# Optimization experiments

Hardware: AMD Instinct MI355X
Metric: run time of the kernel (lower is better)

## Reference

```python
import jax, jax.numpy as jnp
import numpy as np

SIZE_IN = 4096
SIZE_OUT = 4096
BATCH = 4096


def setup_inputs() -> dict:
    key = jax.random.key(0)
    k1, k2, k3, k4, k5, k6 = jax.random.split(key, 6)
    mu_in = jax.random.normal(k1, (BATCH, SIZE_IN), dtype=jnp.float32)
    sigma_in = jax.random.uniform(k2, (BATCH, SIZE_IN), dtype=jnp.float32)
    # parameters, initialized as in the torch module
    w_mu = 5e-05 * jax.random.normal(k3, (SIZE_IN, SIZE_OUT), dtype=jnp.float32)
    w_sigma = jax.random.uniform(k4, (SIZE_IN * SIZE_OUT,), dtype=jnp.float32,
                                 minval=-12.0, maxval=-2.2)
    b_mu = 5e-05 * jax.random.normal(k5, (SIZE_OUT,), dtype=jnp.float32)
    b_sigma = jax.random.uniform(k6, (SIZE_OUT,), dtype=jnp.float32,
                                 minval=-12.0, maxval=-10.0)
    return {"mu_in": mu_in, "sigma_in": sigma_in, "w_mu": w_mu,
            "w_sigma": w_sigma, "b_mu": b_mu, "b_sigma": b_sigma}


def reference(mu_in, sigma_in, w_mu, w_sigma, b_mu, b_sigma):
    # mean path: mu_out[b,o] = sum_i mu_in[b,i] * w_mu[i,o] + b_mu[o]
    mu_out = jnp.einsum('bi,io->bo', mu_in, w_mu) + b_mu
    # variance path: x diag(softplus(w_sigma)) x^T, per output feature.
    # Equivalent to (mu_in^2) @ softplus(w_sigma).reshape(size_in, size_out),
    # avoiding the quadratic diag_embed + bmm materialization.
    sigma_w = jax.nn.softplus(w_sigma).reshape(SIZE_IN, SIZE_OUT)
    Sigma_out = jnp.einsum('bi,io->bo', mu_in * mu_in, sigma_w) + jax.nn.softplus(b_sigma)
    # KL loss, verbatim from the torch code
    sp = jax.nn.softplus(w_sigma)
    term1 = SIZE_IN * jnp.log(sp)
    term2 = jnp.sum(jnp.abs(w_mu))
    term3 = SIZE_IN * sp
    kl_loss = -0.5 * jnp.mean(term1 - term2 - term3)
    return (mu_out, Sigma_out, kl_loss)
```

## Files before the change

### kernel.cpp

```cpp
#include <hip/hip_runtime.h>
#include <hip/hip_bf16.h>
#include <math.h>

#define M_BATCH   4096
#define K_IN      4096
#define N_OUT     4096
#define NELEM     16777216

typedef __bf16 bf16;
typedef bf16  bf16x8 __attribute__((ext_vector_type(8)));
typedef float f32x4  __attribute__((ext_vector_type(4)));

__device__ __forceinline__ float softplus_fast(float x) {
    if (x > 15.f) return x;
    const float e = __expf(x);
    if (e < 0.0883f)
        return e * (1.f + e * (-0.5f + e * 0.3333333f));
    return __logf(1.f + e);
}

__device__ __forceinline__ unsigned short f2bf_bits(float x) {
    bf16 b = (bf16)x;
    return __builtin_bit_cast(unsigned short, b);
}

__device__ __forceinline__ void gload_lds16(const void* g, void* l) {
    __builtin_amdgcn_global_load_lds(
        (__attribute__((address_space(1))) void*)g,
        (__attribute__((address_space(3))) void*)l,
        16, 0, 0);
}

__global__ __launch_bounds__(256) void prep_a(const float4* __restrict__ mu,
                                              ushort4* __restrict__ A,
                                              ushort4* __restrict__ A2) {
    const int i = blockIdx.x * 256 + threadIdx.x;
    const float4 v = mu[i];
    ushort4 a, a2;
    a.x  = f2bf_bits(v.x);       a.y  = f2bf_bits(v.y);
    a.z  = f2bf_bits(v.z);       a.w  = f2bf_bits(v.w);
    a2.x = f2bf_bits(v.x * v.x); a2.y = f2bf_bits(v.y * v.y);
    a2.z = f2bf_bits(v.z * v.z); a2.w = f2bf_bits(v.w * v.w);
    A[i]  = a;
    A2[i] = a2;
}

__global__ __launch_bounds__(256) void prep_w(const float* __restrict__ wmu,
                                              const float* __restrict__ wsg,
                                              bf16* __restrict__ Wmu_t,
                                              bf16* __restrict__ Wsg_t,
                                              float* __restrict__ partials) {
    __shared__ bf16 tmu[64][65];
    __shared__ bf16 tsg[64][65];
    __shared__ float red[256];

    const int t  = threadIdx.x;
    const int ti = blockIdx.y;
    const int tj = blockIdx.x;
    const int r  = t >> 4;
    const int c4 = (t & 15) << 2;

    float s_abs = 0.f, s_sp = 0.f, s_log = 0.f;

    for (int rr = 0; rr < 64; rr += 16) {
        const int row = rr + r;
        const size_t goff = (size_t)(ti * 64 + row) * N_OUT + tj * 64 + c4;
        const float4 vm = *(const float4*)(wmu + goff);
        const float4 vs = *(const float4*)(wsg + goff);
        const float sp0 = softplus_fast(vs.x), sp1 = softplus_fast(vs.y);
        const float sp2 = softplus_fast(vs.z), sp3 = softplus_fast(vs.w);
        s_abs += fabsf(vm.x) + fabsf(vm.y) + fabsf(vm.z) + fabsf(vm.w);
        s_sp  += sp0 + sp1 + sp2 + sp3;
        s_log += __logf(sp0) + __logf(sp1) + __logf(sp2) + __logf(sp3);
        tmu[row][c4 + 0] = (bf16)vm.x; tmu[row][c4 + 1] = (bf16)vm.y;
        tmu[row][c4 + 2] = (bf16)vm.z; tmu[row][c4 + 3] = (bf16)vm.w;
        tsg[row][c4 + 0] = (bf16)sp0;  tsg[row][c4 + 1] = (bf16)sp1;
        tsg[row][c4 + 2] = (bf16)sp2;  tsg[row][c4 + 3] = (bf16)sp3;
    }
    __syncthreads();

    for (int cc = 0; cc < 64; cc += 16) {
        const int j  = cc + r;
        const int i0 = c4;
        ushort4 om, os;
        om.x = __builtin_bit_cast(unsigned short, tmu[i0 + 0][j]);
        om.y = __builtin_bit_cast(unsigned short, tmu[i0 + 1][j]);
        om.z = __builtin_bit_cast(unsigned short, tmu[i0 + 2][j]);
        om.w = __builtin_bit_cast(unsigned short, tmu[i0 + 3][j]);
        os.x = __builtin_bit_cast(unsigned short, tsg[i0 + 0][j]);
        os.y = __builtin_bit_cast(unsigned short, tsg[i0 + 1][j]);
        os.z = __builtin_bit_cast(unsigned short, tsg[i0 + 2][j]);
        os.w = __builtin_bit_cast(unsigned short, tsg[i0 + 3][j]);
        const size_t o = (size_t)(tj * 64 + j) * K_IN + ti * 64 + i0;
        *(ushort4*)(Wmu_t + o) = om;
        *(ushort4*)(Wsg_t + o) = os;
    }

    const int bid = blockIdx.y * 64 + blockIdx.x;
    float vals[3] = { s_log, s_sp, s_abs };
    for (int v = 0; v < 3; v++) {
        __syncthreads();
        red[t] = vals[v];
        __syncthreads();
        for (int s = 128; s > 0; s >>= 1) {
            if (t < s) red[t] += red[t + s];
            __syncthreads();
        }
        if (t == 0) partials[v * 4096 + bid] = red[0];
    }
}

#define MFMA_BF16 __builtin_amdgcn_mfma_f32_16x16x32_bf16

__global__ __launch_bounds__(512, 2) void gemm_bf16(
    const bf16* __restrict__ A1,  const bf16* __restrict__ Bt1,
    const float* __restrict__ bias1, float* __restrict__ C1,
    const bf16* __restrict__ A2_, const bf16* __restrict__ Bt2,
    const float* __restrict__ bias2, float* __restrict__ C2) {

    __shared__ bf16 As[2 * 256 * 64];
    __shared__ bf16 Bs[2 * 256 * 64];

    const int z = blockIdx.z;
    const bf16*  A    = z ? A2_   : A1;
    const bf16*  Bt   = z ? Bt2   : Bt1;
    const float* bias = z ? bias2 : bias1;
    float*       C    = z ? C2    : C1;

    const int t = threadIdx.x;
    const int id   = blockIdx.y * 16 + blockIdx.x;
    const int xcd  = id & 7, cc_ = id >> 3;
    const int rowBase = (((xcd >> 1) << 2) + (cc_ >> 3)) << 8;
    const int colBase = (((xcd & 1) << 3) + (cc_ & 7)) << 8;

    const int srow   = t >> 3;
    const int schunk = (t & 7) ^ (srow & 7);
    const char* aG = (const char*)(A  + (size_t)(rowBase + srow) * K_IN + schunk * 8);
    const char* bG = (const char*)(Bt + (size_t)(colBase + srow) * K_IN + schunk * 8);
    char* aL = (char*)As + t * 16;
    char* bL = (char*)Bs + t * 16;

#define STAGE_A(kt, h, par) do {                                               \
        const size_t kb_ = (size_t)((kt) & 63) << 7;                           \
        gload_lds16(aG + kb_ + (size_t)(h) * (128 * K_IN * 2),                 \
                    aL + ((par) << 15) + ((h) << 14));                         \
        gload_lds16(aG + kb_ + (size_t)(h) * (128 * K_IN * 2) + 64 * K_IN * 2, \
                    aL + ((par) << 15) + ((h) << 14) + 8192);                  \
    } while (0)
#define STAGE_B(kt, h, par) do {                                               \
        const size_t kb_ = (size_t)((kt) & 63) << 7;                           \
        gload_lds16(bG + kb_ + (size_t)(h) * (128 * K_IN * 2),                 \
                    bL + ((par) << 15) + ((h) << 14));                         \
        gload_lds16(bG + kb_ + (size_t)(h) * (128 * K_IN * 2) + 64 * K_IN * 2, \
                    bL + ((par) << 15) + ((h) << 14) + 8192);                  \
    } while (0)

    const int lane = t & 63;
    const int wave = t >> 6;
    const int wr = wave >> 2;
    const int wc = wave & 3;
    const int frow = lane & 15;
    const int blk0 = (lane >> 4) ^ (lane & 7);
    const int c0 = blk0 << 4;
    const int c1 = (blk0 ^ 4) << 4;
    const char* aRd = (const char*)As + ((wr << 7) + frow) * 128;
    const char* bRd = (const char*)Bs + ((wc << 6) + frow) * 128;

#define DS_A(par, fi, ck) (*(const bf16x8*)(aRd + ((par) << 15) + ((fi) << 11) + (ck)))
#define DS_B(par, n,  ck) (*(const bf16x8*)(bRd + ((par) << 15) + ((n)  << 11) + (ck)))

#define PHASE(par, q, STAGE_STMT, VM, BAR) do {                                   \
        if ((q) == 0) {                                                           \
            _Pragma("unroll")                                                     \
            for (int n = 0; n < 4; ++n) {                                         \
                bfrag[n][0] = DS_B(par, n, c0);                                   \
                bfrag[n][1] = DS_B(par, n, c1);                                   \
            }                                                                     \
        }                                                                         \
        const bf16x8 a0k0 = DS_A(par, (q) * 2 + 0, c0);                           \
        const bf16x8 a0k1 = DS_A(par, (q) * 2 + 0, c1);                           \
        const bf16x8 a1k0 = DS_A(par, (q) * 2 + 1, c0);                           \
        const bf16x8 a1k1 = DS_A(par, (q) * 2 + 1, c1);                           \
        STAGE_STMT;                                                               \
        __builtin_amdgcn_s_setprio(1);                                            \
        _Pragma("unroll")                                                         \
        for (int n = 0; n < 4; ++n) {          \
            acc[(q)*2+0][n] = MFMA_BF16(a0k0, bfrag[n][0], acc[(q)*2+0][n],0,0,0);\
            acc[(q)*2+1][n] = MFMA_BF16(a1k0, bfrag[n][0], acc[(q)*2+1][n],0,0,0);\
        }                                                                         \
        _Pragma("unroll")                                                         \
        for (int n = 0; n < 4; ++n) {               \
            acc[(q)*2+0][n] = MFMA_BF16(a0k1, bfrag[n][1], acc[(q)*2+0][n],0,0,0);\
            acc[(q)*2+1][n] = MFMA_BF16(a1k1, bfrag[n][1], acc[(q)*2+1][n],0,0,0);\
        }                                                                         \
        __builtin_amdgcn_s_setprio(0);                                            \
        if (VM) {                                                                 \
            asm volatile("s_waitcnt vmcnt(4)" ::: "memory");                      \
            __builtin_amdgcn_sched_barrier(0);                                    \
        }                                                                         \
        if (BAR) {                                                                \
            __builtin_amdgcn_sched_barrier(0);                                    \
            __builtin_amdgcn_s_barrier();                                         \
            __builtin_amdgcn_sched_barrier(0);                                    \
        }                                                                         \
    } while (0)

    const f32x4 zero = { 0.f, 0.f, 0.f, 0.f };
    f32x4 acc[8][4];
#pragma unroll
    for (int m = 0; m < 8; ++m)
#pragma unroll
        for (int n = 0; n < 4; ++n) acc[m][n] = zero;

    STAGE_A(0, 0, 0); STAGE_A(0, 1, 0);
    STAGE_B(0, 0, 0); STAGE_B(0, 1, 0);
    STAGE_A(1, 0, 1); STAGE_A(1, 1, 1);
    STAGE_B(1, 0, 1); STAGE_B(1, 1, 1);
    asm volatile("s_waitcnt vmcnt(8)" ::: "memory");
    __builtin_amdgcn_sched_barrier(0);
    __builtin_amdgcn_s_barrier();
    __builtin_amdgcn_sched_barrier(0);

    for (int i = 0; i < 32; ++i) {
        const int kA1 = 2 * i + 1;
        const int kB0 = 2 * i + 2;
        const int kA0 = 2 * i + 2;
        const int kB1 = 2 * i + 3;
        {
            bf16x8 bfrag[4][2];
            PHASE(0, 0, STAGE_A(kA1, 0, 1), 0, 0);
            PHASE(0, 1, STAGE_A(kA1, 1, 1), 0, 1);
            PHASE(0, 2, STAGE_B(kB0, 0, 0), 0, 0);
            PHASE(0, 3, STAGE_B(kB0, 1, 0), 1, 1);
        }
        {
            bf16x8 bfrag[4][2];
            PHASE(1, 0, STAGE_A(kA0, 0, 0), 0, 0);
            PHASE(1, 1, STAGE_A(kA0, 1, 0), 0, 1);
            PHASE(1, 2, STAGE_B(kB1, 0, 1), 0, 0);
            PHASE(1, 3, STAGE_B(kB1, 1, 1), 1, 1);
        }
    }

    asm volatile("s_waitcnt vmcnt(0)" ::: "memory");

    const int r0 = (lane >> 4) << 2;
    const int ccol = colBase + (wc << 6) + (lane & 15);
#pragma unroll
    for (int n = 0; n < 4; ++n) {
        const int c = ccol + n * 16;
        float b = bias[c];
        if (z) b = softplus_fast(b);
#pragma unroll
        for (int m = 0; m < 8; ++m) {
            const int rbase = rowBase + (wr << 7) + (m << 4) + r0;
#pragma unroll
            for (int reg = 0; reg < 4; ++reg)
                C[(size_t)(rbase + reg) * N_OUT + c] = acc[m][n][reg] + b;
        }
    }
#undef STAGE_A
#undef STAGE_B
#undef DS_A
#undef DS_B
#undef PHASE
}

__global__ __launch_bounds__(256) void kl_finish(const float* __restrict__ partials,
                                                 const int n,
                                                 float* __restrict__ out) {
    __shared__ double red[256];
    const int t = threadIdx.x;
    double sums[3];
    for (int v = 0; v < 3; v++) {
        double a = 0.0;
        for (int i = t; i < n; i += 256) a += (double)partials[v * n + i];
        red[t] = a;
        __syncthreads();
        for (int s = 128; s > 0; s >>= 1) {
            if (t < s) red[t] += red[t + s];
            __syncthreads();
        }
        sums[v] = red[0];
        __syncthreads();
    }
    if (t == 0) {
        const double mean_log = sums[0] / 16777216.0;
        const double mean_sp  = sums[1] / 16777216.0;
        const double kl = -0.5 * (4096.0 * mean_log - sums[2] - 4096.0 * mean_sp);
        out[0] = (float)kl;
    }
}

__global__ void fb_partials(const float* __restrict__ wmu,
                            const float* __restrict__ wsg,
                            float* __restrict__ partials) {
    __shared__ float red[256];
    const int t = threadIdx.x;
    float s_abs = 0.f, s_sp = 0.f, s_log = 0.f;
    for (int i = blockIdx.x * 256 + t; i < NELEM; i += 1024 * 256) {
        s_abs += fabsf(wmu[i]);
        const float sp = softplus_fast(wsg[i]);
        s_sp += sp;
        s_log += __logf(sp);
    }
    float vals[3] = { s_log, s_sp, s_abs };
    for (int v = 0; v < 3; v++) {
        __syncthreads();
        red[t] = vals[v];
        __syncthreads();
        for (int s = 128; s > 0; s >>= 1) {
            if (t < s) red[t] += red[t + s];
            __syncthreads();
        }
        if (t == 0) partials[v * 1024 + blockIdx.x] = red[0];
    }
}

__global__ void fb_gemm(const float* __restrict__ A,
                        const float* __restrict__ Wm,
                        const float* __restrict__ Ws,
                        const float* __restrict__ bmu,
                        const float* __restrict__ bsg,
                        float* __restrict__ Cmu,
                        float* __restrict__ Csg) {
    __shared__ float As_[16][17], Bm[16][17], Bs_[16][17];
    const int tx = threadIdx.x, ty = threadIdx.y;
    const int row = blockIdx.y * 16 + ty;
    const int col = blockIdx.x * 16 + tx;
    float am = 0.f, as = 0.f;
    for (int k0 = 0; k0 < K_IN; k0 += 16) {
        As_[ty][tx] = A[(size_t)row * K_IN + k0 + tx];
        Bm[ty][tx]  = Wm[(size_t)(k0 + ty) * N_OUT + col];
        Bs_[ty][tx] = softplus_fast(Ws[(size_t)(k0 + ty) * N_OUT + col]);
        __syncthreads();
#pragma unroll
        for (int kk = 0; kk < 16; kk++) {
            const float av = As_[ty][kk];
            am += av * Bm[kk][tx];
            as += av * av * Bs_[kk][tx];
        }
        __syncthreads();
    }
    Cmu[(size_t)row * N_OUT + col] = am + bmu[col];
    Csg[(size_t)row * N_OUT + col] = as + softplus_fast(bsg[col]);
}

extern "C" void kernel_launch(void* const* d_in, const int* in_sizes, int n_in,
                              void* d_out, int out_size, void* d_ws, size_t ws_size,
                              hipStream_t stream) {
    const float* mu_in   = (const float*)d_in[0];
    const float* w_mu    = (const float*)d_in[2];
    const float* w_sigma = (const float*)d_in[3];
    const float* b_mu    = (const float*)d_in[4];
    const float* b_sigma = (const float*)d_in[5];

    float* out_mu  = (float*)d_out;
    float* out_sig = out_mu + (size_t)NELEM;
    float* out_kl  = out_mu + 2 * (size_t)NELEM;

    const size_t mat  = (size_t)NELEM;
    const size_t need = mat * 2 * 4  + 3 * 4096 * sizeof(float);

    if (ws_size >= need) {
        bf16* A      = (bf16*)d_ws;
        bf16* A2     = A + mat;
        bf16* Wmu_t  = A2 + mat;
        bf16* Wsg_t  = Wmu_t + mat;
        float* parts = (float*)(Wsg_t + mat);

        prep_a<<<NELEM / 4 / 256, 256, 0, stream>>>(
            (const float4*)mu_in, (ushort4*)A, (ushort4*)A2);
        prep_w<<<dim3(64, 64), 256, 0, stream>>>(
            w_mu, w_sigma, Wmu_t, Wsg_t, parts);
        gemm_bf16<<<dim3(16, 16, 2), 512, 0, stream>>>(
            A, Wmu_t, b_mu, out_mu, A2, Wsg_t, b_sigma, out_sig);
        kl_finish<<<1, 256, 0, stream>>>(parts, 4096, out_kl);
    } else {
        float* parts = (float*)d_ws;
        fb_partials<<<1024, 256, 0, stream>>>(w_mu, w_sigma, parts);
        fb_gemm<<<dim3(256, 256), dim3(16, 16), 0, stream>>>(
            mu_in, w_mu, w_sigma, b_mu, b_sigma, out_mu, out_sig);
        kl_finish<<<1, 256, 0, stream>>>(parts, 1024, out_kl);
    }
}
```

Before: 575.7 us.

## Switch GEMM to 32x32x16 MFMA and merge prep kernels into one launch

The GEMM inner loop moves from 16x16x32 bf16 MFMA tiles to 32x32x16 tiles. This halves the instruction count per tile and changes the LDS fragment reads and swizzle to match the new operand layout. The two prep kernels (activation cast and weight transpose/softplus) become one launch with the blocks split by index, and the block reduction now uses wavefront shuffles instead of a shared-memory tree. The risk is LDS bank conflicts under the new swizzle and strided epilogue stores.

```diff
diff --git a/kernel.cpp b/kernel.cpp
--- a/kernel.cpp
+++ b/kernel.cpp
@@ -10,6 +10,7 @@
 typedef __bf16 bf16;
 typedef bf16  bf16x8 __attribute__((ext_vector_type(8)));
 typedef float f32x4  __attribute__((ext_vector_type(4)));
+typedef float f32x16 __attribute__((ext_vector_type(16)));
 
 __device__ __forceinline__ float softplus_fast(float x) {
     if (x > 15.f) return x;
@@ -31,32 +32,40 @@
         16, 0, 0);
 }
 
-__global__ __launch_bounds__(256) void prep_a(const float4* __restrict__ mu,
-                                              ushort4* __restrict__ A,
-                                              ushort4* __restrict__ A2) {
-    const int i = blockIdx.x * 256 + threadIdx.x;
-    const float4 v = mu[i];
-    ushort4 a, a2;
-    a.x  = f2bf_bits(v.x);       a.y  = f2bf_bits(v.y);
-    a.z  = f2bf_bits(v.z);       a.w  = f2bf_bits(v.w);
-    a2.x = f2bf_bits(v.x * v.x); a2.y = f2bf_bits(v.y * v.y);
-    a2.z = f2bf_bits(v.z * v.z); a2.w = f2bf_bits(v.w * v.w);
-    A[i]  = a;
-    A2[i] = a2;
-}
-
-__global__ __launch_bounds__(256) void prep_w(const float* __restrict__ wmu,
-                                              const float* __restrict__ wsg,
-                                              bf16* __restrict__ Wmu_t,
-                                              bf16* __restrict__ Wsg_t,
-                                              float* __restrict__ partials) {
+__global__ __launch_bounds__(256) void prep_all(const float* __restrict__ wmu,
+                                                const float* __restrict__ wsg,
+                                                bf16* __restrict__ Wmu_t,
+                                                bf16* __restrict__ Wsg_t,
+                                                float* __restrict__ partials,
+                                                const float4* __restrict__ mu,
+                                                ushort4* __restrict__ A,
+                                                ushort4* __restrict__ A2) {
     __shared__ bf16 tmu[64][65];
     __shared__ bf16 tsg[64][65];
-    __shared__ float red[256];
-
-    const int t  = threadIdx.x;
-    const int ti = blockIdx.y;
-    const int tj = blockIdx.x;
+    __shared__ float wred[4][3];
+
+    const int t   = threadIdx.x;
+    const int bid = blockIdx.x;
+
+    if (bid >= 4096) {
+        const int base = (bid - 4096) * 256 + t;
+#pragma unroll
+        for (int h = 0; h < 2; ++h) {
+            const int i = base + h * 2097152;
+            const float4 v = mu[i];
+            ushort4 a, a2;
+            a.x  = f2bf_bits(v.x);       a.y  = f2bf_bits(v.y);
+            a.z  = f2bf_bits(v.z);       a.w  = f2bf_bits(v.w);
+            a2.x = f2bf_bits(v.x * v.x); a2.y = f2bf_bits(v.y * v.y);
+            a2.z = f2bf_bits(v.z * v.z); a2.w = f2bf_bits(v.w * v.w);
+            A[i]  = a;
+            A2[i] = a2;
+        }
+        return;
+    }
+
+    const int ti = bid >> 6;
+    const int tj = bid & 63;
     const int r  = t >> 4;
     const int c4 = (t & 15) << 2;
 
@@ -96,21 +105,25 @@
         *(ushort4*)(Wsg_t + o) = os;
     }
 
-    const int bid = blockIdx.y * 64 + blockIdx.x;
-    float vals[3] = { s_log, s_sp, s_abs };
-    for (int v = 0; v < 3; v++) {
-        __syncthreads();
-        red[t] = vals[v];
-        __syncthreads();
-        for (int s = 128; s > 0; s >>= 1) {
-            if (t < s) red[t] += red[t + s];
-            __syncthreads();
-        }
-        if (t == 0) partials[v * 4096 + bid] = red[0];
-    }
-}
-
-#define MFMA_BF16 __builtin_amdgcn_mfma_f32_16x16x32_bf16
+    float v0 = s_log, v1 = s_sp, v2 = s_abs;
+#pragma unroll
+    for (int off = 32; off; off >>= 1) {
+        v0 += __shfl_xor(v0, off, 64);
+        v1 += __shfl_xor(v1, off, 64);
+        v2 += __shfl_xor(v2, off, 64);
+    }
+    if ((t & 63) == 0) {
+        wred[t >> 6][0] = v0; wred[t >> 6][1] = v1; wred[t >> 6][2] = v2;
+    }
+    __syncthreads();
+    if (t == 0) {
+        partials[0 * 4096 + bid] = wred[0][0] + wred[1][0] + wred[2][0] + wred[3][0];
+        partials[1 * 4096 + bid] = wred[0][1] + wred[1][1] + wred[2][1] + wred[3][1];
+        partials[2 * 4096 + bid] = wred[0][2] + wred[1][2] + wred[2][2] + wred[3][2];
+    }
+}
+
+#define MFMA32 __builtin_amdgcn_mfma_f32_32x32x16_bf16
 
 __global__ __launch_bounds__(512, 2) void gemm_bf16(
     const bf16* __restrict__ A1,  const bf16* __restrict__ Bt1,
@@ -159,58 +172,54 @@
     const int wave = t >> 6;
     const int wr = wave >> 2;
     const int wc = wave & 3;
-    const int frow = lane & 15;
-    const int blk0 = (lane >> 4) ^ (lane & 7);
-    const int c0 = blk0 << 4;
-    const int c1 = (blk0 ^ 4) << 4;
-    const char* aRd = (const char*)As + ((wr << 7) + frow) * 128;
-    const char* bRd = (const char*)Bs + ((wc << 6) + frow) * 128;
-
-#define DS_A(par, fi, ck) (*(const bf16x8*)(aRd + ((par) << 15) + ((fi) << 11) + (ck)))
-#define DS_B(par, n,  ck) (*(const bf16x8*)(bRd + ((par) << 15) + ((n)  << 11) + (ck)))
-
-#define PHASE(par, q, STAGE_STMT, VM, BAR) do {                                   \
-        if ((q) == 0) {                                                           \
-            _Pragma("unroll")                                                     \
-            for (int n = 0; n < 4; ++n) {                                         \
-                bfrag[n][0] = DS_B(par, n, c0);                                   \
-                bfrag[n][1] = DS_B(par, n, c1);                                   \
-            }                                                                     \
-        }                                                                         \
-        const bf16x8 a0k0 = DS_A(par, (q) * 2 + 0, c0);                           \
-        const bf16x8 a0k1 = DS_A(par, (q) * 2 + 0, c1);                           \
-        const bf16x8 a1k0 = DS_A(par, (q) * 2 + 1, c0);                           \
-        const bf16x8 a1k1 = DS_A(par, (q) * 2 + 1, c1);                           \
-        STAGE_STMT;                                                               \
-        __builtin_amdgcn_s_setprio(1);                                            \
-        _Pragma("unroll")                                                         \
-        for (int n = 0; n < 4; ++n) {          \
-            acc[(q)*2+0][n] = MFMA_BF16(a0k0, bfrag[n][0], acc[(q)*2+0][n],0,0,0);\
-            acc[(q)*2+1][n] = MFMA_BF16(a1k0, bfrag[n][0], acc[(q)*2+1][n],0,0,0);\
-        }                                                                         \
-        _Pragma("unroll")                                                         \
-        for (int n = 0; n < 4; ++n) {               \
-            acc[(q)*2+0][n] = MFMA_BF16(a0k1, bfrag[n][1], acc[(q)*2+0][n],0,0,0);\
-            acc[(q)*2+1][n] = MFMA_BF16(a1k1, bfrag[n][1], acc[(q)*2+1][n],0,0,0);\
-        }                                                                         \
-        __builtin_amdgcn_s_setprio(0);                                            \
-        if (VM) {                                                                 \
-            asm volatile("s_waitcnt vmcnt(4)" ::: "memory");                      \
-            __builtin_amdgcn_sched_barrier(0);                                    \
-        }                                                                         \
-        if (BAR) {                                                                \
-            __builtin_amdgcn_sched_barrier(0);                                    \
-            __builtin_amdgcn_s_barrier();                                         \
-            __builtin_amdgcn_sched_barrier(0);                                    \
-        }                                                                         \
+    const int fr = lane & 31;
+    const int kh = lane >> 5;
+    int cS[4];
+#pragma unroll
+    for (int s = 0; s < 4; ++s)
+        cS[s] = (((s << 1) | kh) ^ (fr & 7)) << 4;
+    const char* aRd = (const char*)As + ((wr << 7) + fr) * 128;
+    const char* bRd = (const char*)Bs + ((wc << 6) + fr) * 128;
+
+#define PHASE(par, q, STAGE_STMT, VM, BAR) do {                                \
+        if ((q) == 0) {                                                        \
+            _Pragma("unroll")                                                  \
+            for (int n = 0; n < 2; ++n)                                        \
+                _Pragma("unroll")                                              \
+                for (int s = 0; s < 4; ++s)                                    \
+                    bfrag[n][s] = *(const bf16x8*)(bRd + ((par) << 15)         \
+                                                  + (n << 12) + cS[s]);        \
+        }                                                                      \
+        bf16x8 a_[4];                                                          \
+        _Pragma("unroll")                                                      \
+        for (int s = 0; s < 4; ++s)                                            \
+            a_[s] = *(const bf16x8*)(aRd + ((par) << 15) + ((q) << 12) + cS[s]);\
+        STAGE_STMT;                                                            \
+        __builtin_amdgcn_s_setprio(1);                                         \
+        _Pragma("unroll")                                                      \
+        for (int s = 0; s < 4; ++s) {                                          \
+            acc[q][0] = MFMA32(a_[s], bfrag[0][s], acc[q][0], 0, 0, 0);        \
+            acc[q][1] = MFMA32(a_[s], bfrag[1][s], acc[q][1], 0, 0, 0);        \
+        }                                                                      \
+        __builtin_amdgcn_s_setprio(0);                                         \
+        if (VM) {                                                              \
+            asm volatile("s_waitcnt vmcnt(4)" ::: "memory");                   \
+            __builtin_amdgcn_sched_barrier(0);                                 \
+        }                                                                      \
+        if (BAR) {                                                             \
+            __builtin_amdgcn_sched_barrier(0);                                 \
+            __builtin_amdgcn_s_barrier();                                      \
+            __builtin_amdgcn_sched_barrier(0);                                 \
+        }                                                                      \
     } while (0)
 
-    const f32x4 zero = { 0.f, 0.f, 0.f, 0.f };
-    f32x4 acc[8][4];
-#pragma unroll
-    for (int m = 0; m < 8; ++m)
-#pragma unroll
-        for (int n = 0; n < 4; ++n) acc[m][n] = zero;
+    f32x16 acc[4][2];
+#pragma unroll
+    for (int m = 0; m < 4; ++m)
+#pragma unroll
+        for (int n = 0; n < 2; ++n)
+#pragma unroll
+            for (int e = 0; e < 16; ++e) acc[m][n][e] = 0.f;
 
     STAGE_A(0, 0, 0); STAGE_A(0, 1, 0);
     STAGE_B(0, 0, 0); STAGE_B(0, 1, 0);
@@ -227,14 +236,14 @@
         const int kA0 = 2 * i + 2;
         const int kB1 = 2 * i + 3;
         {
-            bf16x8 bfrag[4][2];
+            bf16x8 bfrag[2][4];
             PHASE(0, 0, STAGE_A(kA1, 0, 1), 0, 0);
             PHASE(0, 1, STAGE_A(kA1, 1, 1), 0, 1);
             PHASE(0, 2, STAGE_B(kB0, 0, 0), 0, 0);
             PHASE(0, 3, STAGE_B(kB0, 1, 0), 1, 1);
         }
         {
-            bf16x8 bfrag[4][2];
+            bf16x8 bfrag[2][4];
             PHASE(1, 0, STAGE_A(kA0, 0, 0), 0, 0);
             PHASE(1, 1, STAGE_A(kA0, 1, 0), 0, 1);
             PHASE(1, 2, STAGE_B(kB1, 0, 1), 0, 0);
@@ -244,25 +253,23 @@
 
     asm volatile("s_waitcnt vmcnt(0)" ::: "memory");
 
-    const int r0 = (lane >> 4) << 2;
-    const int ccol = colBase + (wc << 6) + (lane & 15);
-#pragma unroll
-    for (int n = 0; n < 4; ++n) {
-        const int c = ccol + n * 16;
+#pragma unroll
+    for (int n = 0; n < 2; ++n) {
+        const int c = colBase + (wc << 6) + (n << 5) + fr;
         float b = bias[c];
         if (z) b = softplus_fast(b);
 #pragma unroll
-        for (int m = 0; m < 8; ++m) {
-            const int rbase = rowBase + (wr << 7) + (m << 4) + r0;
-#pragma unroll
-            for (int reg = 0; reg < 4; ++reg)
-                C[(size_t)(rbase + reg) * N_OUT + c] = acc[m][n][reg] + b;
+        for (int m = 0; m < 4; ++m) {
+            const int rb = rowBase + (wr << 7) + (m << 5) + (kh << 2);
+#pragma unroll
+            for (int reg = 0; reg < 16; ++reg) {
+                const int row = rb + (reg & 3) + ((reg >> 2) << 3);
+                C[(size_t)row * N_OUT + c] = acc[m][n][reg] + b;
+            }
         }
     }
 #undef STAGE_A
 #undef STAGE_B
-#undef DS_A
-#undef DS_B
 #undef PHASE
 }
 
@@ -369,10 +376,9 @@
         bf16* Wsg_t  = Wmu_t + mat;
         float* parts = (float*)(Wsg_t + mat);
 
-        prep_a<<<NELEM / 4 / 256, 256, 0, stream>>>(
+        prep_all<<<4096 + 8192, 256, 0, stream>>>(
+            w_mu, w_sigma, Wmu_t, Wsg_t, parts,
             (const float4*)mu_in, (ushort4*)A, (ushort4*)A2);
-        prep_w<<<dim3(64, 64), 256, 0, stream>>>(
-            w_mu, w_sigma, Wmu_t, Wsg_t, parts);
         gemm_bf16<<<dim3(16, 16, 2), 512, 0, stream>>>(
             A, Wmu_t, b_mu, out_mu, A2, Wsg_t, b_sigma, out_sig);
         kl_finish<<<1, 256, 0, stream>>>(parts, 4096, out_kl);
```

Measured after the change: 573.3 us. About the same (-0.4%).
